# Optimization experiments

Hardware: AMD Instinct MI355X
Metric: run time of the kernel (lower is better)

Reference implementation:

```python
import jax, jax.numpy as jnp
import numpy as np

N_NODES = 1_000_000
EMB_DIM = 128
BATCH = 65536
N_NEG = 20
EPS = 1e-9


def setup_inputs() -> dict:
    key = jax.random.key(0)
    k1, k2, k3, k4, k5 = jax.random.split(key, 5)
    # Xavier-uniform bound for an (N, D) embedding matrix
    bound = float(np.sqrt(6.0 / (N_NODES + EMB_DIM)))
    center_w = jax.random.uniform(k1, (N_NODES, EMB_DIM), jnp.float32, -bound, bound)
    context_w = jax.random.uniform(k2, (N_NODES, EMB_DIM), jnp.float32, -bound, bound)
    center_nodes = jax.random.randint(k3, (BATCH,), 0, N_NODES, dtype=jnp.int64 if jax.config.jax_enable_x64 else jnp.int32)
    context_nodes = jax.random.randint(k4, (BATCH,), 0, N_NODES, dtype=center_nodes.dtype)
    negative_nodes = jax.random.randint(k5, (BATCH, N_NEG), 0, N_NODES, dtype=center_nodes.dtype)
    return {
        "center_nodes": center_nodes,
        "context_nodes": context_nodes,
        "negative_nodes": negative_nodes,
        "center_w": center_w,
        "context_w": context_w,
    }


def reference(center_nodes, context_nodes, negative_nodes, center_w, context_w):
    center_emb = center_w[center_nodes]          # [B, D]
    context_emb = context_w[context_nodes]       # [B, D]
    negative_emb = context_w[negative_nodes]     # [B, K, D]

    pos_score = jnp.sum(center_emb * context_emb, axis=1)          # [B]
    pos_loss = -jnp.log(jax.nn.sigmoid(pos_score) + EPS)           # [B]

    neg_score = jnp.einsum("bkd,bd->bk", negative_emb, center_emb)  # [B, K]
    neg_loss = -jnp.sum(jnp.log(jax.nn.sigmoid(-neg_score) + EPS), axis=1)  # [B]

    return jnp.mean(pos_loss + neg_loss)
```

## Files before the change

### kernel.cpp

```cpp
#include <hip/hip_runtime.h>


constexpr int NNEG = 20;
constexpr int D = 128;
constexpr float EPS = 1e-9f;
constexpr int NBLOCKS = 2048;

__global__ __launch_bounds__(256) void n2v_loss_kernel(
    const int* __restrict__ center_nodes,
    const int* __restrict__ context_nodes,
    const int* __restrict__ negative_nodes,
    const float* __restrict__ center_w,
    const float* __restrict__ context_w,
    float* __restrict__ block_partials,
    int batch)
{
    const int lane  = threadIdx.x & 63;
    const int wave  = threadIdx.x >> 6;
    const int wpb   = blockDim.x >> 6;
    const int gwave = blockIdx.x * wpb + wave;
    const int nwav  = gridDim.x * wpb;

    float acc = 0.0f;

    for (int b = gwave; b < batch; b += nwav) {
        const int ci = center_nodes[b];
        const int xi = context_nodes[b];

        const float2* crow = reinterpret_cast<const float2*>(center_w  + (size_t)ci * D);
        const float2* xrow = reinterpret_cast<const float2*>(context_w + (size_t)xi * D);
        const float2  ce = crow[lane];
        const float2  xe = xrow[lane];

        float sc[NNEG + 1];
        sc[0] = fmaf(ce.x, xe.x, ce.y * xe.y);

        const int* nb = negative_nodes + (size_t)b * NNEG;
#pragma unroll
        for (int k = 0; k < NNEG; ++k) {
            const float2* nrow =
                reinterpret_cast<const float2*>(context_w + (size_t)nb[k] * D);
            const float2 ne = nrow[lane];
            sc[k + 1] = fmaf(ce.x, ne.x, ce.y * ne.y);
        }

#pragma unroll
        for (int k = 0; k <= NNEG; ++k) {
            float v = sc[k];
#pragma unroll
            for (int off = 32; off > 0; off >>= 1)
                v += __shfl_xor(v, off, 64);
            sc[k] = v;
        }

        float loss = -__logf(1.0f / (1.0f + __expf(-sc[0])) + EPS);
#pragma unroll
        for (int k = 1; k <= NNEG; ++k)
            loss -= __logf(1.0f / (1.0f + __expf(sc[k])) + EPS);

        acc += loss;
    }

    __shared__ float wsum[8];
    if (lane == 0) wsum[wave] = acc;
    __syncthreads();
    if (threadIdx.x == 0) {
        float s = 0.0f;
        for (int w = 0; w < wpb; ++w) s += wsum[w];
        block_partials[blockIdx.x] = s;
    }
}

__global__ __launch_bounds__(256) void n2v_reduce_kernel(
    const float* __restrict__ partials, int n, float inv_batch,
    float* __restrict__ out)
{
    __shared__ float sm[256];
    float v = 0.0f;
    for (int i = threadIdx.x; i < n; i += 256) v += partials[i];
    sm[threadIdx.x] = v;
    __syncthreads();
    for (int s = 128; s > 0; s >>= 1) {
        if (threadIdx.x < s) sm[threadIdx.x] += sm[threadIdx.x + s];
        __syncthreads();
    }
    if (threadIdx.x == 0) out[0] = sm[0] * inv_batch;
}

extern "C" void kernel_launch(void* const* d_in, const int* in_sizes, int n_in,
                              void* d_out, int out_size, void* d_ws, size_t ws_size,
                              hipStream_t stream) {
    const int*   center_nodes   = (const int*)d_in[0];
    const int*   context_nodes  = (const int*)d_in[1];
    const int*   negative_nodes = (const int*)d_in[2];
    const float* center_w       = (const float*)d_in[3];
    const float* context_w      = (const float*)d_in[4];
    float*       out            = (float*)d_out;
    const int    batch          = in_sizes[0];

    float* partials = (float*)d_ws;

    n2v_loss_kernel<<<NBLOCKS, 256, 0, stream>>>(
        center_nodes, context_nodes, negative_nodes,
        center_w, context_w, partials, batch);

    n2v_reduce_kernel<<<1, 256, 0, stream>>>(
        partials, NBLOCKS, 1.0f / (float)batch, out);
}
```

Measured before the change: 125.6 us.

## Process two batch rows per wavefront with float4 loads and half-wave reductions

Result: faster. 118.1 us (-5.9%).

```diff
diff --git a/kernel.cpp b/kernel.cpp
--- a/kernel.cpp
+++ b/kernel.cpp
@@ -15,51 +15,70 @@
     float* __restrict__ block_partials,
     int batch)
 {
-    const int lane  = threadIdx.x & 63;
-    const int wave  = threadIdx.x >> 6;
-    const int wpb   = blockDim.x >> 6;
-    const int gwave = blockIdx.x * wpb + wave;
-    const int nwav  = gridDim.x * wpb;
+    const int lane    = threadIdx.x & 63;
+    const int half    = lane >> 5;
+    const int sublane = lane & 31;
+    const int wave    = threadIdx.x >> 6;
+    const int wpb     = blockDim.x >> 6;
+    const int gwave   = blockIdx.x * wpb + wave;
+    const int nwav    = gridDim.x * wpb;
 
     float acc = 0.0f;
 
-    for (int b = gwave; b < batch; b += nwav) {
-        const int ci = center_nodes[b];
-        const int xi = context_nodes[b];
+    for (int b0 = gwave * 2; b0 < batch; b0 += nwav * 2) {
+        const int b = b0 + half;
+        float loss = 0.0f;
 
-        const float2* crow = reinterpret_cast<const float2*>(center_w  + (size_t)ci * D);
-        const float2* xrow = reinterpret_cast<const float2*>(context_w + (size_t)xi * D);
-        const float2  ce = crow[lane];
-        const float2  xe = xrow[lane];
+        if (b < batch) {
+            const int ci = center_nodes[b];
+            const int xi = context_nodes[b];
 
-        float sc[NNEG + 1];
-        sc[0] = fmaf(ce.x, xe.x, ce.y * xe.y);
+            const float4* crow = reinterpret_cast<const float4*>(center_w  + (size_t)ci * D);
+            const float4* xrow = reinterpret_cast<const float4*>(context_w + (size_t)xi * D);
+            const float4  ce = crow[sublane];
+            const float4  xe = xrow[sublane];
 
-        const int* nb = negative_nodes + (size_t)b * NNEG;
+            int nb[NNEG];
+            {
+                const int4* np4 = reinterpret_cast<const int4*>(negative_nodes + (size_t)b * NNEG);
 #pragma unroll
-        for (int k = 0; k < NNEG; ++k) {
-            const float2* nrow =
-                reinterpret_cast<const float2*>(context_w + (size_t)nb[k] * D);
-            const float2 ne = nrow[lane];
-            sc[k + 1] = fmaf(ce.x, ne.x, ce.y * ne.y);
-        }
+                for (int q = 0; q < 5; ++q) {
+                    const int4 v = np4[q];
+                    nb[q * 4 + 0] = v.x; nb[q * 4 + 1] = v.y;
+                    nb[q * 4 + 2] = v.z; nb[q * 4 + 3] = v.w;
+                }
+            }
+
+            float sc[NNEG + 1];
+            sc[0] = fmaf(ce.x, xe.x, fmaf(ce.y, xe.y, fmaf(ce.z, xe.z, ce.w * xe.w)));
 
 #pragma unroll
-        for (int k = 0; k <= NNEG; ++k) {
-            float v = sc[k];
+            for (int k = 0; k < NNEG; ++k) {
+                const float4* nrow =
+                    reinterpret_cast<const float4*>(context_w + (size_t)nb[k] * D);
+                const float4 ne = nrow[sublane];
+                sc[k + 1] = fmaf(ce.x, ne.x, fmaf(ce.y, ne.y, fmaf(ce.z, ne.z, ce.w * ne.w)));
+            }
+
 #pragma unroll
-            for (int off = 32; off > 0; off >>= 1)
-                v += __shfl_xor(v, off, 64);
-            sc[k] = v;
+            for (int k = 0; k <= NNEG; ++k) {
+                float v = sc[k];
+#pragma unroll
+                for (int off = 16; off > 0; off >>= 1)
+                    v += __shfl_xor(v, off, 64);
+                sc[k] = v;
+            }
+
+            loss = -__logf(1.0f / (1.0f + __expf(-sc[0])) + EPS);
+#pragma unroll
+            for (int k = 1; k <= NNEG; ++k)
+                loss -= __logf(1.0f / (1.0f + __expf(sc[k])) + EPS);
         }
-
-        float loss = -__logf(1.0f / (1.0f + __expf(-sc[0])) + EPS);
-#pragma unroll
-        for (int k = 1; k <= NNEG; ++k)
-            loss -= __logf(1.0f / (1.0f + __expf(sc[k])) + EPS);
 
         acc += loss;
     }
+
+    acc += __shfl_xor(acc, 32, 64);
 
     __shared__ float wsum[8];
     if (lane == 0) wsum[wave] = acc;
```
